# Optimization experiments

Hardware: AMD Instinct MI355X
Metric: run time of the kernel (lower is better)

The kernel has to match this reference:

```python
import jax, jax.numpy as jnp
import numpy as np

N = 100000   # nodes
E = 1600000  # edges (before self-loops)
F = 128      # num_features
H = 128      # hidden_dim
EPS = 1e-5   # BatchNorm eps


def setup_inputs() -> dict:
    key = jax.random.key(0)
    ks = jax.random.split(key, 8)
    x = jax.random.normal(ks[0], (N, F), dtype=jnp.float32)
    edge_index = jax.random.randint(ks[1], (2, E), 0, N, dtype=jnp.int64)

    def lin(k, din, dout):
        s = 1.0 / np.sqrt(din)
        kw, kb = jax.random.split(k)
        W = jax.random.uniform(kw, (din, dout), jnp.float32, -s, s)
        b = jax.random.uniform(kb, (dout,), jnp.float32, -s, s)
        return W, b

    W1, b1 = lin(ks[2], F, H)
    W2, b2 = lin(ks[3], H, H)
    W3, b3 = lin(ks[4], H, H)
    Wc, bc = lin(ks[5], H, 2)

    def bn_params():
        return (jnp.ones((H,), jnp.float32), jnp.zeros((H,), jnp.float32),
                jnp.zeros((H,), jnp.float32), jnp.ones((H,), jnp.float32))

    g1, be1, rm1, rv1 = bn_params()
    g2, be2, rm2, rv2 = bn_params()
    g3, be3, rm3, rv3 = bn_params()

    return {"x": x, "edge_index": edge_index,
            "W1": W1, "b1": b1, "W2": W2, "b2": b2, "W3": W3, "b3": b3,
            "g1": g1, "be1": be1, "rm1": rm1, "rv1": rv1,
            "g2": g2, "be2": be2, "rm2": rm2, "rv2": rv2,
            "g3": g3, "be3": be3, "rm3": rm3, "rv3": rv3,
            "Wc": Wc, "bc": bc}


def _gcn_norm(edge_index, num_nodes):
    # add self-loops, compute symmetric normalization (PyG GCNConv default)
    loop = jnp.arange(num_nodes, dtype=edge_index.dtype)
    src = jnp.concatenate([edge_index[0], loop])
    dst = jnp.concatenate([edge_index[1], loop])
    deg = jax.ops.segment_sum(jnp.ones_like(dst, dtype=jnp.float32), dst,
                              num_segments=num_nodes)
    dinv = jnp.where(deg > 0, jax.lax.rsqrt(deg), 0.0)
    norm = dinv[src] * dinv[dst]  # [E+N]
    return src, dst, norm


def _gcn_conv(x, W, b, src, dst, norm, num_nodes):
    h = x @ W                              # [N, H] linear first
    msg = h[src] * norm[:, None]           # gather + scale  [E+N, H]
    out = jax.ops.segment_sum(msg, dst, num_segments=num_nodes)  # scatter-add
    return out + b


def _bn_eval(x, g, be, rm, rv):
    return (x - rm) * jax.lax.rsqrt(rv + EPS) * g + be


def reference(x, edge_index,
              W1, b1, W2, b2, W3, b3,
              g1, be1, rm1, rv1,
              g2, be2, rm2, rv2,
              g3, be3, rm3, rv3,
              Wc, bc):
    n = x.shape[0]
    src, dst, norm = _gcn_norm(edge_index, n)
    h = _gcn_conv(x, W1, b1, src, dst, norm, n)
    h = _bn_eval(jax.nn.relu(h), g1, be1, rm1, rv1)
    # dropout: identity in eval mode
    h = _gcn_conv(h, W2, b2, src, dst, norm, n)
    h = _bn_eval(jax.nn.relu(h), g2, be2, rm2, rv2)
    h = _gcn_conv(h, W3, b3, src, dst, norm, n)
    h = _bn_eval(jax.nn.relu(h), g3, be3, rm3, rv3)
    return h @ Wc + bc  # [N, 2]
```

## Files before the change

### kernel.cpp

```cpp
#include <hip/hip_runtime.h>
#include <hip/hip_fp16.h>

#define BN_EPS 1e-5f
#define CHUNK 4096

typedef _Float16 half8 __attribute__((ext_vector_type(8)));
typedef float f32x4 __attribute__((ext_vector_type(4)));

__device__ __forceinline__ float4 f4zero() { return make_float4(0.f, 0.f, 0.f, 0.f); }


__global__ __launch_bounds__(256) void k_bucket_hist(const int* __restrict__ dst,
                                                     int* __restrict__ tableT,
                                                     int nA, int nbuck, int e) {
    __shared__ int h[1024];
    int blk = blockIdx.x, tid = threadIdx.x;
    for (int k = tid; k < 1024; k += 256) h[k] = 0;
    __syncthreads();
    int base = blk * CHUNK;
    if (base + CHUNK <= e && (e & 3) == 0) {
        const int4* d4 = (const int4*)(dst + base);
#pragma unroll
        for (int t = 0; t < 4; ++t) {
            int4 d = d4[t * 256 + tid];
            atomicAdd(&h[d.x >> 8], 1);
            atomicAdd(&h[d.y >> 8], 1);
            atomicAdd(&h[d.z >> 8], 1);
            atomicAdd(&h[d.w >> 8], 1);
        }
    } else {
        for (int i = base + tid; i < e && i < base + CHUNK; i += 256)
            atomicAdd(&h[dst[i] >> 8], 1);
    }
    __syncthreads();
    for (int k = tid; k < nbuck; k += 256)
        tableT[(size_t)k * nA + blk] = h[k];
}

__global__ __launch_bounds__(256) void k_bucket_scatter(const int* __restrict__ src,
                                                        const int* __restrict__ dst,
                                                        const int* __restrict__ tableT,
                                                        int2* __restrict__ bed,
                                                        int nA, int nbuck, int e) {
    __shared__ int cur[1024];
    int blk = blockIdx.x, tid = threadIdx.x;
    for (int k = tid; k < nbuck; k += 256)
        cur[k] = tableT[(size_t)k * nA + blk];
    __syncthreads();
    int base = blk * CHUNK;
    if (base + CHUNK <= e && (e & 3) == 0) {
        const int4* s4 = (const int4*)(src + base);
        const int4* d4 = (const int4*)(dst + base);
#pragma unroll
        for (int t = 0; t < 4; ++t) {
            int4 s = s4[t * 256 + tid];
            int4 d = d4[t * 256 + tid];
            int p0 = atomicAdd(&cur[d.x >> 8], 1); bed[p0] = make_int2(s.x, d.x);
            int p1 = atomicAdd(&cur[d.y >> 8], 1); bed[p1] = make_int2(s.y, d.y);
            int p2 = atomicAdd(&cur[d.z >> 8], 1); bed[p2] = make_int2(s.z, d.z);
            int p3 = atomicAdd(&cur[d.w >> 8], 1); bed[p3] = make_int2(s.w, d.w);
        }
    } else {
        for (int i = base + tid; i < e && i < base + CHUNK; i += 256) {
            int d = dst[i];
            int p = atomicAdd(&cur[d >> 8], 1);
            bed[p] = make_int2(src[i], d);
        }
    }
}

__global__ __launch_bounds__(256) void k_bucket_rank(const int2* __restrict__ bed,
                                                     const int* __restrict__ tableT,
                                                     int* __restrict__ brank,
                                                     int* __restrict__ counts,
                                                     int nA, int nbuck, int n, int e) {
    __shared__ int lcnt[256];
    int b = blockIdx.x, tid = threadIdx.x;
    lcnt[tid] = 0;
    __syncthreads();
    int start = tableT[(size_t)b * nA];
    int end = (b + 1 < nbuck) ? tableT[(size_t)(b + 1) * nA] : e;
    for (int i = start + tid; i < end; i += 256) {
        int2 q = bed[i];
        brank[i] = atomicAdd(&lcnt[q.y & 255], 1);
    }
    __syncthreads();
    int node = (b << 8) + tid;
    if (node < n) counts[node] = lcnt[tid];
}

__global__ __launch_bounds__(256) void k_dinv(const int* __restrict__ counts,
                                              float* __restrict__ dinv, int n) {
    int i = blockIdx.x * 256 + threadIdx.x;
    if (i < n) dinv[i] = rsqrtf((float)(counts[i] + 1));
}

template <bool PAD8>
__global__ __launch_bounds__(1024) void k_scan_block(const int* __restrict__ counts,
                                                     int* __restrict__ offs,
                                                     int* __restrict__ partials, int len) {
    __shared__ int s[1024];
    int t = threadIdx.x;
    int gid = blockIdx.x * 1024 + t;
    int c = (gid < len) ? counts[gid] : 0;
    int v = PAD8 ? ((c + 7) & ~7) : c;
    int x = v;
    s[t] = x;
    __syncthreads();
    for (int d = 1; d < 1024; d <<= 1) {
        int y = (t >= d) ? s[t - d] : 0;
        __syncthreads();
        x += y;
        s[t] = x;
        __syncthreads();
    }
    if (gid < len) offs[gid] = x - v;
    if (t == 1023) partials[blockIdx.x] = x;
}

__global__ __launch_bounds__(1024) void k_scan_partials(int* __restrict__ partials, int nb) {
    __shared__ int s[1024];
    int t = threadIdx.x;
    int v = (t < nb) ? partials[t] : 0;
    int x = v;
    s[t] = x;
    __syncthreads();
    for (int d = 1; d < 1024; d <<= 1) {
        int y = (t >= d) ? s[t - d] : 0;
        __syncthreads();
        x += y;
        s[t] = x;
        __syncthreads();
    }
    if (t < nb) partials[t] = x - v;
    if (t == nb - 1) partials[nb] = x;
}

__global__ __launch_bounds__(256) void k_scan_add(int* __restrict__ offs,
                                                  const int* __restrict__ partials, int len) {
    int gid = blockIdx.x * 256 + threadIdx.x;
    if (gid < len) offs[gid] += partials[gid >> 10];
    if (gid == 0) offs[len] = partials[(len + 1023) >> 10];
}

__global__ __launch_bounds__(256) void k_fill(int4* __restrict__ er4, int val, int m4) {
    int i = blockIdx.x * 256 + threadIdx.x;
    if (i < m4) er4[i] = make_int4(val, val, val, val);
}

__global__ __launch_bounds__(256) void k_place2(const int2* __restrict__ bed,
                                                const int* __restrict__ brank,
                                                const int* __restrict__ offs,
                                                int* __restrict__ er, int e) {
    int i = (blockIdx.x * 256 + threadIdx.x) * 2;
    if (i + 1 < e) {
        int4 q = *(const int4*)(bed + i);
        int2 r = *(const int2*)(brank + i);
        er[offs[q.y] + r.x] = q.x;
        er[offs[q.w] + r.y] = q.z;
    } else if (i < e) {
        int2 q = bed[i];
        er[offs[q.y] + brank[i]] = q.x;
    }
}


__global__ __launch_bounds__(256) void k_packW(const float* __restrict__ W,
                                               _Float16* __restrict__ out) {
    int t = blockIdx.x * 256 + threadIdx.x;
    if (t >= 2048) return;
    int kc = t >> 9;
    int rem = t & 511;
    int ct = rem >> 6;
    int lane = rem & 63;
    int q = lane >> 4;
    int col = ct * 16 + (lane & 15);
    half8 h;
#pragma unroll
    for (int j = 0; j < 8; ++j)
        h[j] = (_Float16)W[(kc * 32 + q * 8 + j) * 128 + col];
    *(half8*)(out + (size_t)t * 8) = h;
}


template <bool AF32>
__global__ __launch_bounds__(256) void k_gemm_mfma(const void* __restrict__ Av,
                                                   const _Float16* __restrict__ pW,
                                                   const float* __restrict__ dinv,
                                                   uint4* __restrict__ C, int n) {
    __shared__ char smem[32768];
    uint4* sW = (uint4*)smem;
    int tid = threadIdx.x;

    {
        const uint4* gW = (const uint4*)pW;
#pragma unroll
        for (int i = 0; i < 8; ++i) sW[tid + 256 * i] = gW[tid + 256 * i];
    }
    __syncthreads();

    int wave = tid >> 6, lane = tid & 63;
    int quad = lane >> 4, l16 = lane & 15;
    int row0 = blockIdx.x * 64 + wave * 16;
    int arow = row0 + l16;
    int arowc = (arow < n) ? arow : (n - 1);

    half8 af[4];
    if (AF32) {
        const float* A = (const float*)Av + (size_t)arowc * 128 + quad * 8;
#pragma unroll
        for (int kc = 0; kc < 4; ++kc) {
            float4 lo = *(const float4*)(A + kc * 32);
            float4 hi = *(const float4*)(A + kc * 32 + 4);
            half8 h;
            h[0] = (_Float16)lo.x; h[1] = (_Float16)lo.y;
            h[2] = (_Float16)lo.z; h[3] = (_Float16)lo.w;
            h[4] = (_Float16)hi.x; h[5] = (_Float16)hi.y;
            h[6] = (_Float16)hi.z; h[7] = (_Float16)hi.w;
            af[kc] = h;
        }
    } else {
        const _Float16* A = (const _Float16*)Av + (size_t)arowc * 128 + quad * 8;
#pragma unroll
        for (int kc = 0; kc < 4; ++kc)
            af[kc] = *(const half8*)(A + kc * 32);
    }

    f32x4 acc[8];
#pragma unroll
    for (int ct = 0; ct < 8; ++ct) acc[ct] = (f32x4){0.f, 0.f, 0.f, 0.f};

#pragma unroll
    for (int kc = 0; kc < 4; ++kc) {
#pragma unroll
        for (int ct = 0; ct < 8; ++ct) {
            half8 bf = *(half8*)&sW[(kc * 8 + ct) * 64 + lane];
            acc[ct] = __builtin_amdgcn_mfma_f32_16x16x32_f16(af[kc], bf, acc[ct], 0, 0, 0);
        }
    }

    __syncthreads();

    _Float16* eb = (_Float16*)smem + wave * 16 * 136;
    float dv[4];
#pragma unroll
    for (int r = 0; r < 4; ++r) {
        int rr = row0 + quad * 4 + r;
        dv[r] = dinv[(rr < n) ? rr : (n - 1)];
    }
#pragma unroll
    for (int ct = 0; ct < 8; ++ct)
#pragma unroll
        for (int r = 0; r < 4; ++r)
            eb[(quad * 4 + r) * 136 + ct * 16 + l16] = (_Float16)(acc[ct][r] * dv[r]);

#pragma unroll
    for (int i = 0; i < 4; ++i) {
        int linear = i * 64 + lane;
        int r = linear >> 4, c = linear & 15;
        uint4 v = *(uint4*)((char*)eb + r * 272 + c * 16);
        int row = row0 + r;
        if (row < n) C[(size_t)row * 16 + c] = v;
    }
}


__device__ __forceinline__ void acc_row(float4& acc, uint2 q) {
    float2 f01 = __half22float2(*(__half2*)&q.x);
    float2 f23 = __half22float2(*(__half2*)&q.y);
    acc.x += f01.x; acc.y += f01.y; acc.z += f23.x; acc.w += f23.y;
}

template <bool FUSE_CLS>
__global__ __launch_bounds__(256) void k_aggregate(const uint2* __restrict__ Ah,
                                                   const int* __restrict__ offs,
                                                   const int* __restrict__ er,
                                                   const float* __restrict__ dinv,
                                                   const float* __restrict__ bias,
                                                   const float* __restrict__ g,
                                                   const float* __restrict__ be,
                                                   const float* __restrict__ rm,
                                                   const float* __restrict__ rv,
                                                   uint2* __restrict__ Hout,
                                                   const float* __restrict__ Wc,
                                                   const float* __restrict__ bc,
                                                   float* __restrict__ out, int n) {
    int lane = threadIdx.x & 31;
    int node = blockIdx.x * 8 + (threadIdx.x >> 5);
    if (node >= n) return;

    float4 acc = f4zero();
    acc_row(acc, Ah[node * 32 + lane]);

    int e0 = offs[node], e1 = offs[node + 1];
    for (int e = e0; e < e1; e += 8) {
        int4 ra = *(const int4*)(er + e);
        int4 rb = *(const int4*)(er + e + 4);
        uint2 v0 = Ah[ra.x * 32 + lane];
        uint2 v1 = Ah[ra.y * 32 + lane];
        uint2 v2 = Ah[ra.z * 32 + lane];
        uint2 v3 = Ah[ra.w * 32 + lane];
        uint2 v4 = Ah[rb.x * 32 + lane];
        uint2 v5 = Ah[rb.y * 32 + lane];
        uint2 v6 = Ah[rb.z * 32 + lane];
        uint2 v7 = Ah[rb.w * 32 + lane];
        acc_row(acc, v0); acc_row(acc, v1); acc_row(acc, v2); acc_row(acc, v3);
        acc_row(acc, v4); acc_row(acc, v5); acc_row(acc, v6); acc_row(acc, v7);
    }

    float di = dinv[node];
    acc.x *= di; acc.y *= di; acc.z *= di; acc.w *= di;

    float4 b4  = ((const float4*)bias)[lane];
    float4 g4  = ((const float4*)g)[lane];
    float4 be4 = ((const float4*)be)[lane];
    float4 rm4 = ((const float4*)rm)[lane];
    float4 rv4 = ((const float4*)rv)[lane];

    float4 o;
    float v;
    v = fmaxf(acc.x + b4.x, 0.f); o.x = (v - rm4.x) * rsqrtf(rv4.x + BN_EPS) * g4.x + be4.x;
    v = fmaxf(acc.y + b4.y, 0.f); o.y = (v - rm4.y) * rsqrtf(rv4.y + BN_EPS) * g4.y + be4.y;
    v = fmaxf(acc.z + b4.z, 0.f); o.z = (v - rm4.z) * rsqrtf(rv4.z + BN_EPS) * g4.z + be4.z;
    v = fmaxf(acc.w + b4.w, 0.f); o.w = (v - rm4.w) * rsqrtf(rv4.w + BN_EPS) * g4.w + be4.w;

    if (!FUSE_CLS) {
        __half2 p0 = __floats2half2_rn(o.x, o.y);
        __half2 p1 = __floats2half2_rn(o.z, o.w);
        uint2 u;
        u.x = *(unsigned int*)&p0;
        u.y = *(unsigned int*)&p1;
        Hout[node * 32 + lane] = u;
    } else {
        const float4* Wv = (const float4*)Wc;
        float4 w01 = Wv[2 * lane];
        float4 w23 = Wv[2 * lane + 1];
        float p0 = o.x * w01.x + o.y * w01.z + o.z * w23.x + o.w * w23.z;
        float p1 = o.x * w01.y + o.y * w01.w + o.z * w23.y + o.w * w23.w;
#pragma unroll
        for (int d = 16; d >= 1; d >>= 1) {
            p0 += __shfl_down(p0, d, 32);
            p1 += __shfl_down(p1, d, 32);
        }
        if (lane == 0) {
            out[node * 2 + 0] = p0 + bc[0];
            out[node * 2 + 1] = p1 + bc[1];
        }
    }
}


extern "C" void kernel_launch(void* const* d_in, const int* in_sizes, int n_in,
                              void* d_out, int out_size, void* d_ws, size_t ws_size,
                              hipStream_t stream) {
    const float* x   = (const float*)d_in[0];
    const int*   ei  = (const int*)d_in[1];
    const float* W1  = (const float*)d_in[2];
    const float* b1  = (const float*)d_in[3];
    const float* W2  = (const float*)d_in[4];
    const float* b2  = (const float*)d_in[5];
    const float* W3  = (const float*)d_in[6];
    const float* b3  = (const float*)d_in[7];
    const float* g1  = (const float*)d_in[8];
    const float* be1 = (const float*)d_in[9];
    const float* rm1 = (const float*)d_in[10];
    const float* rv1 = (const float*)d_in[11];
    const float* g2  = (const float*)d_in[12];
    const float* be2 = (const float*)d_in[13];
    const float* rm2 = (const float*)d_in[14];
    const float* rv2 = (const float*)d_in[15];
    const float* g3  = (const float*)d_in[16];
    const float* be3 = (const float*)d_in[17];
    const float* rm3 = (const float*)d_in[18];
    const float* rv3 = (const float*)d_in[19];
    const float* Wc  = (const float*)d_in[20];
    const float* bc  = (const float*)d_in[21];
    float* out = (float*)d_out;

    int n = in_sizes[0] / 128;
    int e = in_sizes[1] / 2;
    const int* src = ei;
    const int* dst = ei + e;

    char* ws = (char*)d_ws;
    size_t off = 0;
    auto alloc = [&](size_t bytes) -> char* {
        char* p = ws + off;
        off += (bytes + 255) & ~(size_t)255;
        return p;
    };
    int erCap = e + 8 * n;
    uint2*     bufA   = (uint2*)alloc((size_t)(n + 1) * 128 * 2);
    char*      bufH   = (char*) alloc((size_t)n * 128 * 4);
    float*     dinv   = (float*)alloc((size_t)n * 4);
    int*       counts = (int*)  alloc((size_t)n * 4);
    int*       offs   = (int*)  alloc((size_t)(n + 1) * 4);
    int*       parts  = (int*)  alloc(8192);
    int*       er     = (int*)  alloc((size_t)erCap * 4);
    _Float16*  pW     = (_Float16*)alloc(3 * 16384 * 2);
    (void)ws_size; (void)n_in; (void)out_size;

    int nA    = (e + CHUNK - 1) / CHUNK;
    int nbuck = (n + 255) >> 8;
    int tlen  = nbuck * nA;
    {
        char* p = bufH + (size_t)n * 128 * 2;
        size_t po = 0;
        auto palloc = [&](size_t bytes) -> char* {
            char* q = p + po;
            po += (bytes + 255) & ~(size_t)255;
            return q;
        };
        int2* bed    = (int2*)palloc((size_t)e * 8);
        int*  brank  = (int*) palloc((size_t)e * 4);
        int*  tableT = (int*) palloc((size_t)(tlen + 1) * 4);

        hipMemsetAsync(bufA + (size_t)n * 32, 0, 256, stream);

        int gN  = (n + 255) / 256;
        int nb  = (n + 1023) / 1024;
        int nbT = (tlen + 1023) / 1024;
        int m4  = erCap / 4;

        k_packW<<<8, 256, 0, stream>>>(W1, pW);
        k_packW<<<8, 256, 0, stream>>>(W2, pW + 16384);
        k_packW<<<8, 256, 0, stream>>>(W3, pW + 32768);
        k_bucket_hist<<<nA, 256, 0, stream>>>(dst, tableT, nA, nbuck, e);
        k_scan_block<false><<<nbT, 1024, 0, stream>>>(tableT, tableT, parts, tlen);
        k_scan_partials<<<1, 1024, 0, stream>>>(parts, nbT);
        k_scan_add<<<(tlen + 255) / 256, 256, 0, stream>>>(tableT, parts, tlen);
        k_bucket_scatter<<<nA, 256, 0, stream>>>(src, dst, tableT, bed, nA, nbuck, e);
        k_bucket_rank<<<nbuck, 256, 0, stream>>>(bed, tableT, brank, counts, nA, nbuck, n, e);
        k_dinv<<<gN, 256, 0, stream>>>(counts, dinv, n);
        k_scan_block<true><<<nb, 1024, 0, stream>>>(counts, offs, parts, n);
        k_scan_partials<<<1, 1024, 0, stream>>>(parts, nb);
        k_scan_add<<<gN, 256, 0, stream>>>(offs, parts, n);
        k_fill<<<(m4 + 255) / 256, 256, 0, stream>>>((int4*)er, n, m4);
        k_place2<<<((e + 1) / 2 + 255) / 256, 256, 0, stream>>>(bed, brank, offs, er, e);
    }

    int gGemm = (n + 63) / 64;
    int gAgg  = (n + 7) / 8;

    k_gemm_mfma<true><<<gGemm, 256, 0, stream>>>(x, pW, dinv, (uint4*)bufA, n);
    k_aggregate<false><<<gAgg, 256, 0, stream>>>(bufA, offs, er, dinv,
                                                 b1, g1, be1, rm1, rv1, (uint2*)bufH,
                                                 nullptr, nullptr, nullptr, n);

    k_gemm_mfma<false><<<gGemm, 256, 0, stream>>>(bufH, pW + 16384, dinv, (uint4*)bufA, n);
    k_aggregate<false><<<gAgg, 256, 0, stream>>>(bufA, offs, er, dinv,
                                                 b2, g2, be2, rm2, rv2, (uint2*)bufH,
                                                 nullptr, nullptr, nullptr, n);

    k_gemm_mfma<false><<<gGemm, 256, 0, stream>>>(bufH, pW + 32768, dinv, (uint4*)bufA, n);
    k_aggregate<true><<<gAgg, 256, 0, stream>>>(bufA, offs, er, dinv,
                                                b3, g3, be3, rm3, rv3, nullptr,
                                                Wc, bc, out, n);
}
```

Baseline: 412.2 us.

## Widen aggregate gathers to 16-byte loads with half-wave edge split, shrink buckets

The aggregation kernel now has each 16-lane half-wave load full 16-byte fp16 chunks. The two halves work on alternating edges, and their partial sums are combined with a cross-half shuffle. Accumulation uses fdot2 to convert fp16 to fp32 while adding. Separately, the bucket sort uses 128-node buckets and smaller chunks, and the dinv computation is folded into the rank kernel, which removes one launch. The wider gathers should cut per-edge memory instructions, at the cost of an extra reduction and idle lanes for the self-row and the output store.

```diff
diff --git a/kernel.cpp b/kernel.cpp
--- a/kernel.cpp
+++ b/kernel.cpp
@@ -2,9 +2,11 @@
 #include <hip/hip_fp16.h>
 
 #define BN_EPS 1e-5f
-#define CHUNK 4096
+#define CHUNK 2048
+#define BBITS 7
 
 typedef _Float16 half8 __attribute__((ext_vector_type(8)));
+typedef _Float16 half2v __attribute__((ext_vector_type(2)));
 typedef float f32x4 __attribute__((ext_vector_type(4)));
 
 __device__ __forceinline__ float4 f4zero() { return make_float4(0.f, 0.f, 0.f, 0.f); }
@@ -21,16 +23,16 @@
     if (base + CHUNK <= e && (e & 3) == 0) {
         const int4* d4 = (const int4*)(dst + base);
 #pragma unroll
-        for (int t = 0; t < 4; ++t) {
+        for (int t = 0; t < CHUNK / 1024; ++t) {
             int4 d = d4[t * 256 + tid];
-            atomicAdd(&h[d.x >> 8], 1);
-            atomicAdd(&h[d.y >> 8], 1);
-            atomicAdd(&h[d.z >> 8], 1);
-            atomicAdd(&h[d.w >> 8], 1);
+            atomicAdd(&h[d.x >> BBITS], 1);
+            atomicAdd(&h[d.y >> BBITS], 1);
+            atomicAdd(&h[d.z >> BBITS], 1);
+            atomicAdd(&h[d.w >> BBITS], 1);
         }
     } else {
         for (int i = base + tid; i < e && i < base + CHUNK; i += 256)
-            atomicAdd(&h[dst[i] >> 8], 1);
+            atomicAdd(&h[dst[i] >> BBITS], 1);
     }
     __syncthreads();
     for (int k = tid; k < nbuck; k += 256)
@@ -52,18 +54,18 @@
         const int4* s4 = (const int4*)(src + base);
         const int4* d4 = (const int4*)(dst + base);
 #pragma unroll
-        for (int t = 0; t < 4; ++t) {
+        for (int t = 0; t < CHUNK / 1024; ++t) {
             int4 s = s4[t * 256 + tid];
             int4 d = d4[t * 256 + tid];
-            int p0 = atomicAdd(&cur[d.x >> 8], 1); bed[p0] = make_int2(s.x, d.x);
-            int p1 = atomicAdd(&cur[d.y >> 8], 1); bed[p1] = make_int2(s.y, d.y);
-            int p2 = atomicAdd(&cur[d.z >> 8], 1); bed[p2] = make_int2(s.z, d.z);
-            int p3 = atomicAdd(&cur[d.w >> 8], 1); bed[p3] = make_int2(s.w, d.w);
+            int p0 = atomicAdd(&cur[d.x >> BBITS], 1); bed[p0] = make_int2(s.x, d.x);
+            int p1 = atomicAdd(&cur[d.y >> BBITS], 1); bed[p1] = make_int2(s.y, d.y);
+            int p2 = atomicAdd(&cur[d.z >> BBITS], 1); bed[p2] = make_int2(s.z, d.z);
+            int p3 = atomicAdd(&cur[d.w >> BBITS], 1); bed[p3] = make_int2(s.w, d.w);
         }
     } else {
         for (int i = base + tid; i < e && i < base + CHUNK; i += 256) {
             int d = dst[i];
-            int p = atomicAdd(&cur[d >> 8], 1);
+            int p = atomicAdd(&cur[d >> BBITS], 1);
             bed[p] = make_int2(src[i], d);
         }
     }
@@ -73,26 +75,27 @@
                                                      const int* __restrict__ tableT,
                                                      int* __restrict__ brank,
                                                      int* __restrict__ counts,
+                                                     float* __restrict__ dinv,
                                                      int nA, int nbuck, int n, int e) {
-    __shared__ int lcnt[256];
+    __shared__ int lcnt[128];
     int b = blockIdx.x, tid = threadIdx.x;
-    lcnt[tid] = 0;
+    if (tid < 128) lcnt[tid] = 0;
     __syncthreads();
     int start = tableT[(size_t)b * nA];
     int end = (b + 1 < nbuck) ? tableT[(size_t)(b + 1) * nA] : e;
     for (int i = start + tid; i < end; i += 256) {
         int2 q = bed[i];
-        brank[i] = atomicAdd(&lcnt[q.y & 255], 1);
-    }
-    __syncthreads();
-    int node = (b << 8) + tid;
-    if (node < n) counts[node] = lcnt[tid];
-}
-
-__global__ __launch_bounds__(256) void k_dinv(const int* __restrict__ counts,
-                                              float* __restrict__ dinv, int n) {
-    int i = blockIdx.x * 256 + threadIdx.x;
-    if (i < n) dinv[i] = rsqrtf((float)(counts[i] + 1));
+        brank[i] = atomicAdd(&lcnt[q.y & ((1 << BBITS) - 1)], 1);
+    }
+    __syncthreads();
+    if (tid < 128) {
+        int node = (b << BBITS) + tid;
+        if (node < n) {
+            int c = lcnt[tid];
+            counts[node] = c;
+            dinv[node] = rsqrtf((float)(c + 1));
+        }
+    }
 }
 
 template <bool PAD8>
@@ -265,14 +268,20 @@
 }
 
 
-__device__ __forceinline__ void acc_row(float4& acc, uint2 q) {
-    float2 f01 = __half22float2(*(__half2*)&q.x);
-    float2 f23 = __half22float2(*(__half2*)&q.y);
-    acc.x += f01.x; acc.y += f01.y; acc.z += f23.x; acc.w += f23.y;
+__device__ __forceinline__ void accum8(float* acc, uint4 q) {
+    const half2v b0 = {(_Float16)1.0f, (_Float16)0.0f};
+    const half2v b1 = {(_Float16)0.0f, (_Float16)1.0f};
+    unsigned int u[4] = {q.x, q.y, q.z, q.w};
+#pragma unroll
+    for (int k = 0; k < 4; ++k) {
+        half2v h = *(half2v*)&u[k];
+        acc[2 * k + 0] = __builtin_amdgcn_fdot2(h, b0, acc[2 * k + 0], false);
+        acc[2 * k + 1] = __builtin_amdgcn_fdot2(h, b1, acc[2 * k + 1], false);
+    }
 }
 
 template <bool FUSE_CLS>
-__global__ __launch_bounds__(256) void k_aggregate(const uint2* __restrict__ Ah,
+__global__ __launch_bounds__(256) void k_aggregate(const uint4* __restrict__ Ah4,
                                                    const int* __restrict__ offs,
                                                    const int* __restrict__ er,
                                                    const float* __restrict__ dinv,
@@ -281,68 +290,88 @@
                                                    const float* __restrict__ be,
                                                    const float* __restrict__ rm,
                                                    const float* __restrict__ rv,
-                                                   uint2* __restrict__ Hout,
+                                                   uint4* __restrict__ Hout,
                                                    const float* __restrict__ Wc,
                                                    const float* __restrict__ bc,
                                                    float* __restrict__ out, int n) {
-    int lane = threadIdx.x & 31;
+    int lane32 = threadIdx.x & 31;
     int node = blockIdx.x * 8 + (threadIdx.x >> 5);
     if (node >= n) return;
-
-    float4 acc = f4zero();
-    acc_row(acc, Ah[node * 32 + lane]);
+    int sub = lane32 & 15;
+    bool hi = lane32 >= 16;
+
+    float acc[8];
+#pragma unroll
+    for (int j = 0; j < 8; ++j) acc[j] = 0.f;
+
+    {
+        uint4 qs = Ah4[(size_t)node * 16 + sub];
+        if (!hi) accum8(acc, qs);
+    }
 
     int e0 = offs[node], e1 = offs[node + 1];
     for (int e = e0; e < e1; e += 8) {
         int4 ra = *(const int4*)(er + e);
         int4 rb = *(const int4*)(er + e + 4);
-        uint2 v0 = Ah[ra.x * 32 + lane];
-        uint2 v1 = Ah[ra.y * 32 + lane];
-        uint2 v2 = Ah[ra.z * 32 + lane];
-        uint2 v3 = Ah[ra.w * 32 + lane];
-        uint2 v4 = Ah[rb.x * 32 + lane];
-        uint2 v5 = Ah[rb.y * 32 + lane];
-        uint2 v6 = Ah[rb.z * 32 + lane];
-        uint2 v7 = Ah[rb.w * 32 + lane];
-        acc_row(acc, v0); acc_row(acc, v1); acc_row(acc, v2); acc_row(acc, v3);
-        acc_row(acc, v4); acc_row(acc, v5); acc_row(acc, v6); acc_row(acc, v7);
-    }
+        int r0 = hi ? ra.y : ra.x;
+        int r1 = hi ? ra.w : ra.z;
+        int r2 = hi ? rb.y : rb.x;
+        int r3 = hi ? rb.w : rb.z;
+        uint4 q0 = Ah4[(size_t)r0 * 16 + sub];
+        uint4 q1 = Ah4[(size_t)r1 * 16 + sub];
+        uint4 q2 = Ah4[(size_t)r2 * 16 + sub];
+        uint4 q3 = Ah4[(size_t)r3 * 16 + sub];
+        accum8(acc, q0); accum8(acc, q1); accum8(acc, q2); accum8(acc, q3);
+    }
+
+#pragma unroll
+    for (int j = 0; j < 8; ++j) acc[j] += __shfl_xor(acc[j], 16, 32);
 
     float di = dinv[node];
-    acc.x *= di; acc.y *= di; acc.z *= di; acc.w *= di;
-
-    float4 b4  = ((const float4*)bias)[lane];
-    float4 g4  = ((const float4*)g)[lane];
-    float4 be4 = ((const float4*)be)[lane];
-    float4 rm4 = ((const float4*)rm)[lane];
-    float4 rv4 = ((const float4*)rv)[lane];
-
-    float4 o;
-    float v;
-    v = fmaxf(acc.x + b4.x, 0.f); o.x = (v - rm4.x) * rsqrtf(rv4.x + BN_EPS) * g4.x + be4.x;
-    v = fmaxf(acc.y + b4.y, 0.f); o.y = (v - rm4.y) * rsqrtf(rv4.y + BN_EPS) * g4.y + be4.y;
-    v = fmaxf(acc.z + b4.z, 0.f); o.z = (v - rm4.z) * rsqrtf(rv4.z + BN_EPS) * g4.z + be4.z;
-    v = fmaxf(acc.w + b4.w, 0.f); o.w = (v - rm4.w) * rsqrtf(rv4.w + BN_EPS) * g4.w + be4.w;
+    const float4* b4 = (const float4*)bias;
+    const float4* g4 = (const float4*)g;
+    const float4* be4 = (const float4*)be;
+    const float4* rm4 = (const float4*)rm;
+    const float4* rv4 = (const float4*)rv;
+
+    float o[8];
+#pragma unroll
+    for (int h = 0; h < 2; ++h) {
+        float4 bb = b4[sub * 2 + h], gg = g4[sub * 2 + h], ee = be4[sub * 2 + h];
+        float4 mm = rm4[sub * 2 + h], vv = rv4[sub * 2 + h];
+        float v;
+        v = fmaxf(acc[4 * h + 0] * di + bb.x, 0.f); o[4 * h + 0] = (v - mm.x) * rsqrtf(vv.x + BN_EPS) * gg.x + ee.x;
+        v = fmaxf(acc[4 * h + 1] * di + bb.y, 0.f); o[4 * h + 1] = (v - mm.y) * rsqrtf(vv.y + BN_EPS) * gg.y + ee.y;
+        v = fmaxf(acc[4 * h + 2] * di + bb.z, 0.f); o[4 * h + 2] = (v - mm.z) * rsqrtf(vv.z + BN_EPS) * gg.z + ee.z;
+        v = fmaxf(acc[4 * h + 3] * di + bb.w, 0.f); o[4 * h + 3] = (v - mm.w) * rsqrtf(vv.w + BN_EPS) * gg.w + ee.w;
+    }
 
     if (!FUSE_CLS) {
-        __half2 p0 = __floats2half2_rn(o.x, o.y);
-        __half2 p1 = __floats2half2_rn(o.z, o.w);
-        uint2 u;
-        u.x = *(unsigned int*)&p0;
-        u.y = *(unsigned int*)&p1;
-        Hout[node * 32 + lane] = u;
+        if (!hi) {
+            __half2 p0 = __floats2half2_rn(o[0], o[1]);
+            __half2 p1 = __floats2half2_rn(o[2], o[3]);
+            __half2 p2 = __floats2half2_rn(o[4], o[5]);
+            __half2 p3 = __floats2half2_rn(o[6], o[7]);
+            uint4 u;
+            u.x = *(unsigned int*)&p0; u.y = *(unsigned int*)&p1;
+            u.z = *(unsigned int*)&p2; u.w = *(unsigned int*)&p3;
+            Hout[(size_t)node * 16 + sub] = u;
+        }
     } else {
         const float4* Wv = (const float4*)Wc;
-        float4 w01 = Wv[2 * lane];
-        float4 w23 = Wv[2 * lane + 1];
-        float p0 = o.x * w01.x + o.y * w01.z + o.z * w23.x + o.w * w23.z;
-        float p1 = o.x * w01.y + o.y * w01.w + o.z * w23.y + o.w * w23.w;
-#pragma unroll
-        for (int d = 16; d >= 1; d >>= 1) {
-            p0 += __shfl_down(p0, d, 32);
-            p1 += __shfl_down(p1, d, 32);
-        }
-        if (lane == 0) {
+        float p0 = 0.f, p1 = 0.f;
+#pragma unroll
+        for (int k = 0; k < 4; ++k) {
+            float4 w = Wv[sub * 4 + k];
+            p0 += o[2 * k] * w.x + o[2 * k + 1] * w.z;
+            p1 += o[2 * k] * w.y + o[2 * k + 1] * w.w;
+        }
+#pragma unroll
+        for (int d = 8; d >= 1; d >>= 1) {
+            p0 += __shfl_down(p0, d, 16);
+            p1 += __shfl_down(p1, d, 16);
+        }
+        if (lane32 == 0) {
             out[node * 2 + 0] = p0 + bc[0];
             out[node * 2 + 1] = p1 + bc[1];
         }
@@ -401,7 +430,7 @@
     (void)ws_size; (void)n_in; (void)out_size;
 
     int nA    = (e + CHUNK - 1) / CHUNK;
-    int nbuck = (n + 255) >> 8;
+    int nbuck = (n + (1 << BBITS) - 1) >> BBITS;
     int tlen  = nbuck * nA;
     {
         char* p = bufH + (size_t)n * 128 * 2;
@@ -430,8 +459,7 @@
         k_scan_partials<<<1, 1024, 0, stream>>>(parts, nbT);
         k_scan_add<<<(tlen + 255) / 256, 256, 0, stream>>>(tableT, parts, tlen);
         k_bucket_scatter<<<nA, 256, 0, stream>>>(src, dst, tableT, bed, nA, nbuck, e);
-        k_bucket_rank<<<nbuck, 256, 0, stream>>>(bed, tableT, brank, counts, nA, nbuck, n, e);
-        k_dinv<<<gN, 256, 0, stream>>>(counts, dinv, n);
+        k_bucket_rank<<<nbuck, 256, 0, stream>>>(bed, tableT, brank, counts, dinv, nA, nbuck, n, e);
         k_scan_block<true><<<nb, 1024, 0, stream>>>(counts, offs, parts, n);
         k_scan_partials<<<1, 1024, 0, stream>>>(parts, nb);
         k_scan_add<<<gN, 256, 0, stream>>>(offs, parts, n);
@@ -443,17 +471,17 @@
     int gAgg  = (n + 7) / 8;
 
     k_gemm_mfma<true><<<gGemm, 256, 0, stream>>>(x, pW, dinv, (uint4*)bufA, n);
-    k_aggregate<false><<<gAgg, 256, 0, stream>>>(bufA, offs, er, dinv,
-                                                 b1, g1, be1, rm1, rv1, (uint2*)bufH,
+    k_aggregate<false><<<gAgg, 256, 0, stream>>>((const uint4*)bufA, offs, er, dinv,
+                                                 b1, g1, be1, rm1, rv1, (uint4*)bufH,
                                                  nullptr, nullptr, nullptr, n);
 
     k_gemm_mfma<false><<<gGemm, 256, 0, stream>>>(bufH, pW + 16384, dinv, (uint4*)bufA, n);
-    k_aggregate<false><<<gAgg, 256, 0, stream>>>(bufA, offs, er, dinv,
-                                                 b2, g2, be2, rm2, rv2, (uint2*)bufH,
+    k_aggregate<false><<<gAgg, 256, 0, stream>>>((const uint4*)bufA, offs, er, dinv,
+                                                 b2, g2, be2, rm2, rv2, (uint4*)bufH,
                                                  nullptr, nullptr, nullptr, n);
 
     k_gemm_mfma<false><<<gGemm, 256, 0, stream>>>(bufH, pW + 32768, dinv, (uint4*)bufA, n);
-    k_aggregate<true><<<gAgg, 256, 0, stream>>>(bufA, offs, er, dinv,
+    k_aggregate<true><<<gAgg, 256, 0, stream>>>((const uint4*)bufA, offs, er, dinv,
                                                 b3, g3, be3, rm3, rv3, nullptr,
                                                 Wc, bc, out, n);
 }
```

Result: slower. 433.8 us (+5.3%).

## Fuse CSR-build preprocessing into fewer kernels with per-bucket local scans

Applied to the files above, without the earlier changes.

Restructures the graph preprocessing pipeline. Weight packing is merged into the histogram kernel, and bucket size shrinks to 128 nodes. The rank kernel now also computes dinv and a padded local prefix scan per bucket, so the global node scan becomes a small scan over bucket totals. The fill, place and zeroing steps are merged into one finalize kernel. This cuts the launch count roughly in half and drops the full-array padding fill, at the cost of more histogram buckets and a serial per-node padding loop.

```diff
diff --git a/kernel.cpp b/kernel.cpp
--- a/kernel.cpp
+++ b/kernel.cpp
@@ -3,6 +3,7 @@
 
 #define BN_EPS 1e-5f
 #define CHUNK 4096
+#define BBITS 7
 
 typedef _Float16 half8 __attribute__((ext_vector_type(8)));
 typedef float f32x4 __attribute__((ext_vector_type(4)));
@@ -10,32 +11,95 @@
 __device__ __forceinline__ float4 f4zero() { return make_float4(0.f, 0.f, 0.f, 0.f); }
 
 
-__global__ __launch_bounds__(256) void k_bucket_hist(const int* __restrict__ dst,
-                                                     int* __restrict__ tableT,
-                                                     int nA, int nbuck, int e) {
+__global__ __launch_bounds__(256) void k_pack_hist(const float* __restrict__ W1,
+                                                   const float* __restrict__ W2,
+                                                   const float* __restrict__ W3,
+                                                   _Float16* __restrict__ pW,
+                                                   const int* __restrict__ dst,
+                                                   int* __restrict__ tableT,
+                                                   int nA, int nbuck, int e) {
     __shared__ int h[1024];
-    int blk = blockIdx.x, tid = threadIdx.x;
+    int tid = threadIdx.x;
+    if (blockIdx.x < 24) {
+        int t = blockIdx.x * 256 + tid;
+        int wi = t >> 11;
+        int tt = t & 2047;
+        const float* W = (wi == 0) ? W1 : ((wi == 1) ? W2 : W3);
+        int kc = tt >> 9;
+        int rem = tt & 511;
+        int ct = rem >> 6;
+        int lane = rem & 63;
+        int q = lane >> 4;
+        int col = ct * 16 + (lane & 15);
+        half8 hh;
+#pragma unroll
+        for (int j = 0; j < 8; ++j)
+            hh[j] = (_Float16)W[(kc * 32 + q * 8 + j) * 128 + col];
+        *(half8*)(pW + (size_t)t * 8) = hh;
+        return;
+    }
+    int blk = blockIdx.x - 24;
     for (int k = tid; k < 1024; k += 256) h[k] = 0;
     __syncthreads();
     int base = blk * CHUNK;
     if (base + CHUNK <= e && (e & 3) == 0) {
         const int4* d4 = (const int4*)(dst + base);
 #pragma unroll
-        for (int t = 0; t < 4; ++t) {
+        for (int t = 0; t < CHUNK / 1024; ++t) {
             int4 d = d4[t * 256 + tid];
-            atomicAdd(&h[d.x >> 8], 1);
-            atomicAdd(&h[d.y >> 8], 1);
-            atomicAdd(&h[d.z >> 8], 1);
-            atomicAdd(&h[d.w >> 8], 1);
+            atomicAdd(&h[d.x >> BBITS], 1);
+            atomicAdd(&h[d.y >> BBITS], 1);
+            atomicAdd(&h[d.z >> BBITS], 1);
+            atomicAdd(&h[d.w >> BBITS], 1);
         }
     } else {
         for (int i = base + tid; i < e && i < base + CHUNK; i += 256)
-            atomicAdd(&h[dst[i] >> 8], 1);
+            atomicAdd(&h[dst[i] >> BBITS], 1);
     }
     __syncthreads();
     for (int k = tid; k < nbuck; k += 256)
         tableT[(size_t)k * nA + blk] = h[k];
 }
+
+
+__global__ __launch_bounds__(1024) void k_scan_block(const int* __restrict__ in,
+                                                     int* __restrict__ outp,
+                                                     int* __restrict__ partials, int len) {
+    __shared__ int s[1024];
+    int t = threadIdx.x;
+    int gid = blockIdx.x * 1024 + t;
+    int v = (gid < len) ? in[gid] : 0;
+    int x = v;
+    s[t] = x;
+    __syncthreads();
+    for (int d = 1; d < 1024; d <<= 1) {
+        int y = (t >= d) ? s[t - d] : 0;
+        __syncthreads();
+        x += y;
+        s[t] = x;
+        __syncthreads();
+    }
+    if (gid < len) outp[gid] = x - v;
+    if (t == 1023) partials[blockIdx.x] = x;
+}
+
+__global__ __launch_bounds__(256) void k_scan_addp(int* __restrict__ data,
+                                                   const int* __restrict__ partials, int len) {
+    __shared__ int red[256];
+    int tid = threadIdx.x;
+    int K = blockIdx.x >> 2;
+    int s = 0;
+    for (int t = tid; t < K; t += 256) s += partials[t];
+    red[tid] = s;
+    __syncthreads();
+    for (int d = 128; d > 0; d >>= 1) {
+        if (tid < d) red[tid] += red[tid + d];
+        __syncthreads();
+    }
+    int gid = blockIdx.x * 256 + tid;
+    if (gid < len) data[gid] += red[0];
+}
+
 
 __global__ __launch_bounds__(256) void k_bucket_scatter(const int* __restrict__ src,
                                                         const int* __restrict__ dst,
@@ -52,58 +116,74 @@
         const int4* s4 = (const int4*)(src + base);
         const int4* d4 = (const int4*)(dst + base);
 #pragma unroll
-        for (int t = 0; t < 4; ++t) {
+        for (int t = 0; t < CHUNK / 1024; ++t) {
             int4 s = s4[t * 256 + tid];
             int4 d = d4[t * 256 + tid];
-            int p0 = atomicAdd(&cur[d.x >> 8], 1); bed[p0] = make_int2(s.x, d.x);
-            int p1 = atomicAdd(&cur[d.y >> 8], 1); bed[p1] = make_int2(s.y, d.y);
-            int p2 = atomicAdd(&cur[d.z >> 8], 1); bed[p2] = make_int2(s.z, d.z);
-            int p3 = atomicAdd(&cur[d.w >> 8], 1); bed[p3] = make_int2(s.w, d.w);
+            int p0 = atomicAdd(&cur[d.x >> BBITS], 1); bed[p0] = make_int2(s.x, d.x);
+            int p1 = atomicAdd(&cur[d.y >> BBITS], 1); bed[p1] = make_int2(s.y, d.y);
+            int p2 = atomicAdd(&cur[d.z >> BBITS], 1); bed[p2] = make_int2(s.z, d.z);
+            int p3 = atomicAdd(&cur[d.w >> BBITS], 1); bed[p3] = make_int2(s.w, d.w);
         }
     } else {
         for (int i = base + tid; i < e && i < base + CHUNK; i += 256) {
             int d = dst[i];
-            int p = atomicAdd(&cur[d >> 8], 1);
+            int p = atomicAdd(&cur[d >> BBITS], 1);
             bed[p] = make_int2(src[i], d);
         }
     }
 }
+
 
 __global__ __launch_bounds__(256) void k_bucket_rank(const int2* __restrict__ bed,
                                                      const int* __restrict__ tableT,
                                                      int* __restrict__ brank,
                                                      int* __restrict__ counts,
+                                                     float* __restrict__ dinv,
+                                                     int* __restrict__ localOff,
+                                                     int* __restrict__ btot,
                                                      int nA, int nbuck, int n, int e) {
-    __shared__ int lcnt[256];
+    __shared__ int lcnt[128];
+    __shared__ int lscan[128];
     int b = blockIdx.x, tid = threadIdx.x;
-    lcnt[tid] = 0;
+    if (tid < 128) lcnt[tid] = 0;
     __syncthreads();
     int start = tableT[(size_t)b * nA];
     int end = (b + 1 < nbuck) ? tableT[(size_t)(b + 1) * nA] : e;
     for (int i = start + tid; i < end; i += 256) {
         int2 q = bed[i];
-        brank[i] = atomicAdd(&lcnt[q.y & 255], 1);
-    }
-    __syncthreads();
-    int node = (b << 8) + tid;
-    if (node < n) counts[node] = lcnt[tid];
-}
-
-__global__ __launch_bounds__(256) void k_dinv(const int* __restrict__ counts,
-                                              float* __restrict__ dinv, int n) {
-    int i = blockIdx.x * 256 + threadIdx.x;
-    if (i < n) dinv[i] = rsqrtf((float)(counts[i] + 1));
-}
-
-template <bool PAD8>
-__global__ __launch_bounds__(1024) void k_scan_block(const int* __restrict__ counts,
-                                                     int* __restrict__ offs,
-                                                     int* __restrict__ partials, int len) {
+        brank[i] = atomicAdd(&lcnt[q.y & 127], 1);
+    }
+    __syncthreads();
+    int padded = 0;
+    if (tid < 128) {
+        padded = (lcnt[tid] + 7) & ~7;
+        lscan[tid] = padded;
+    }
+    __syncthreads();
+    for (int d = 1; d < 128; d <<= 1) {
+        int y = (tid < 128 && tid >= d) ? lscan[tid - d] : 0;
+        __syncthreads();
+        if (tid < 128) lscan[tid] += y;
+        __syncthreads();
+    }
+    if (tid < 128) {
+        int node = (b << BBITS) + tid;
+        if (node < n) {
+            int c = lcnt[tid];
+            counts[node] = c;
+            dinv[node] = rsqrtf((float)(c + 1));
+            localOff[node] = lscan[tid] - padded;
+        }
+        if (tid == 127) btot[b] = lscan[127];
+    }
+}
+
+
+__global__ __launch_bounds__(1024) void k_scan_buckets(const int* __restrict__ btot,
+                                                       int* __restrict__ bucketBase, int nbuck) {
     __shared__ int s[1024];
     int t = threadIdx.x;
-    int gid = blockIdx.x * 1024 + t;
-    int c = (gid < len) ? counts[gid] : 0;
-    int v = PAD8 ? ((c + 7) & ~7) : c;
+    int v = (t < nbuck) ? btot[t] : 0;
     int x = v;
     s[t] = x;
     __syncthreads();
@@ -114,72 +194,44 @@
         s[t] = x;
         __syncthreads();
     }
-    if (gid < len) offs[gid] = x - v;
-    if (t == 1023) partials[blockIdx.x] = x;
-}
-
-__global__ __launch_bounds__(1024) void k_scan_partials(int* __restrict__ partials, int nb) {
-    __shared__ int s[1024];
-    int t = threadIdx.x;
-    int v = (t < nb) ? partials[t] : 0;
-    int x = v;
-    s[t] = x;
-    __syncthreads();
-    for (int d = 1; d < 1024; d <<= 1) {
-        int y = (t >= d) ? s[t - d] : 0;
-        __syncthreads();
-        x += y;
-        s[t] = x;
-        __syncthreads();
-    }
-    if (t < nb) partials[t] = x - v;
-    if (t == nb - 1) partials[nb] = x;
-}
-
-__global__ __launch_bounds__(256) void k_scan_add(int* __restrict__ offs,
-                                                  const int* __restrict__ partials, int len) {
-    int gid = blockIdx.x * 256 + threadIdx.x;
-    if (gid < len) offs[gid] += partials[gid >> 10];
-    if (gid == 0) offs[len] = partials[(len + 1023) >> 10];
-}
-
-__global__ __launch_bounds__(256) void k_fill(int4* __restrict__ er4, int val, int m4) {
-    int i = blockIdx.x * 256 + threadIdx.x;
-    if (i < m4) er4[i] = make_int4(val, val, val, val);
-}
-
-__global__ __launch_bounds__(256) void k_place2(const int2* __restrict__ bed,
-                                                const int* __restrict__ brank,
-                                                const int* __restrict__ offs,
-                                                int* __restrict__ er, int e) {
-    int i = (blockIdx.x * 256 + threadIdx.x) * 2;
-    if (i + 1 < e) {
-        int4 q = *(const int4*)(bed + i);
-        int2 r = *(const int2*)(brank + i);
-        er[offs[q.y] + r.x] = q.x;
-        er[offs[q.w] + r.y] = q.z;
-    } else if (i < e) {
-        int2 q = bed[i];
-        er[offs[q.y] + brank[i]] = q.x;
-    }
-}
-
-
-__global__ __launch_bounds__(256) void k_packW(const float* __restrict__ W,
-                                               _Float16* __restrict__ out) {
-    int t = blockIdx.x * 256 + threadIdx.x;
-    if (t >= 2048) return;
-    int kc = t >> 9;
-    int rem = t & 511;
-    int ct = rem >> 6;
-    int lane = rem & 63;
-    int q = lane >> 4;
-    int col = ct * 16 + (lane & 15);
-    half8 h;
-#pragma unroll
-    for (int j = 0; j < 8; ++j)
-        h[j] = (_Float16)W[(kc * 32 + q * 8 + j) * 128 + col];
-    *(half8*)(out + (size_t)t * 8) = h;
+    if (t < nbuck) bucketBase[t] = x - v;
+    if (t == nbuck - 1) bucketBase[nbuck] = x;
+}
+
+
+__global__ __launch_bounds__(256) void k_finalize(const int* __restrict__ counts,
+                                                  const int* __restrict__ localOff,
+                                                  const int* __restrict__ bucketBase,
+                                                  int* __restrict__ offs,
+                                                  int* __restrict__ er,
+                                                  const int2* __restrict__ bed,
+                                                  const int* __restrict__ brank,
+                                                  unsigned int* __restrict__ bufAzero,
+                                                  int n, int e, int gN, int nbuck) {
+    int tid = threadIdx.x;
+    if (blockIdx.x < gN) {
+        int node = blockIdx.x * 256 + tid;
+        if (node < n) {
+            int c = counts[node];
+            int o = bucketBase[node >> BBITS] + localOff[node];
+            offs[node] = o;
+            int pc = (c + 7) & ~7;
+            for (int j = c; j < pc; ++j) er[o + j] = n;
+        }
+        if (node == 0) offs[n] = bucketBase[nbuck];
+        if (blockIdx.x == 0 && tid < 64) bufAzero[tid] = 0u;
+    } else {
+        int i = ((blockIdx.x - gN) * 256 + tid) * 2;
+        if (i + 1 < e) {
+            int4 q = *(const int4*)(bed + i);
+            int2 r = *(const int2*)(brank + i);
+            er[bucketBase[q.y >> BBITS] + localOff[q.y] + r.x] = q.x;
+            er[bucketBase[q.w >> BBITS] + localOff[q.w] + r.y] = q.z;
+        } else if (i < e) {
+            int2 q = bed[i];
+            er[bucketBase[q.y >> BBITS] + localOff[q.y] + brank[i]] = q.x;
+        }
+    }
 }
 
 
@@ -290,20 +342,20 @@
     if (node >= n) return;
 
     float4 acc = f4zero();
-    acc_row(acc, Ah[node * 32 + lane]);
+    acc_row(acc, Ah[(size_t)node * 32 + lane]);
 
     int e0 = offs[node], e1 = offs[node + 1];
     for (int e = e0; e < e1; e += 8) {
         int4 ra = *(const int4*)(er + e);
         int4 rb = *(const int4*)(er + e + 4);
-        uint2 v0 = Ah[ra.x * 32 + lane];
-        uint2 v1 = Ah[ra.y * 32 + lane];
-        uint2 v2 = Ah[ra.z * 32 + lane];
-        uint2 v3 = Ah[ra.w * 32 + lane];
-        uint2 v4 = Ah[rb.x * 32 + lane];
-        uint2 v5 = Ah[rb.y * 32 + lane];
-        uint2 v6 = Ah[rb.z * 32 + lane];
-        uint2 v7 = Ah[rb.w * 32 + lane];
+        uint2 v0 = Ah[(size_t)ra.x * 32 + lane];
+        uint2 v1 = Ah[(size_t)ra.y * 32 + lane];
+        uint2 v2 = Ah[(size_t)ra.z * 32 + lane];
+        uint2 v3 = Ah[(size_t)ra.w * 32 + lane];
+        uint2 v4 = Ah[(size_t)rb.x * 32 + lane];
+        uint2 v5 = Ah[(size_t)rb.y * 32 + lane];
+        uint2 v6 = Ah[(size_t)rb.z * 32 + lane];
+        uint2 v7 = Ah[(size_t)rb.w * 32 + lane];
         acc_row(acc, v0); acc_row(acc, v1); acc_row(acc, v2); acc_row(acc, v3);
         acc_row(acc, v4); acc_row(acc, v5); acc_row(acc, v6); acc_row(acc, v7);
     }
@@ -330,7 +382,7 @@
         uint2 u;
         u.x = *(unsigned int*)&p0;
         u.y = *(unsigned int*)&p1;
-        Hout[node * 32 + lane] = u;
+        Hout[(size_t)node * 32 + lane] = u;
     } else {
         const float4* Wv = (const float4*)Wc;
         float4 w01 = Wv[2 * lane];
@@ -389,71 +441,57 @@
         off += (bytes + 255) & ~(size_t)255;
         return p;
     };
+    int nA    = (e + CHUNK - 1) / CHUNK;
+    int nbuck = (n + (1 << BBITS) - 1) >> BBITS;
+    int tlen  = nbuck * nA;
     int erCap = e + 8 * n;
-    uint2*     bufA   = (uint2*)alloc((size_t)(n + 1) * 128 * 2);
-    char*      bufH   = (char*) alloc((size_t)n * 128 * 4);
-    float*     dinv   = (float*)alloc((size_t)n * 4);
-    int*       counts = (int*)  alloc((size_t)n * 4);
-    int*       offs   = (int*)  alloc((size_t)(n + 1) * 4);
-    int*       parts  = (int*)  alloc(8192);
-    int*       er     = (int*)  alloc((size_t)erCap * 4);
-    _Float16*  pW     = (_Float16*)alloc(3 * 16384 * 2);
+
+    char*      bufA     = (char*) alloc((size_t)(n + 1) * 256);
+    char*      bufH     = (char*) alloc((size_t)n * 256);
+    float*     dinv     = (float*)alloc((size_t)n * 4);
+    int*       counts   = (int*)  alloc((size_t)n * 4);
+    int*       offs     = (int*)  alloc((size_t)(n + 1) * 4);
+    int*       localOff = (int*)  alloc((size_t)n * 4);
+    int*       btot     = (int*)  alloc((size_t)(nbuck + 1) * 4);
+    int*       bktBase  = (int*)  alloc((size_t)(nbuck + 1) * 4);
+    int*       tableT   = (int*)  alloc((size_t)(tlen + 1) * 4);
+    int*       parts    = (int*)  alloc(8192);
+    int*       er       = (int*)  alloc((size_t)erCap * 4);
+    _Float16*  pW       = (_Float16*)alloc(3 * 16384 * 2);
     (void)ws_size; (void)n_in; (void)out_size;
 
-    int nA    = (e + CHUNK - 1) / CHUNK;
-    int nbuck = (n + 255) >> 8;
-    int tlen  = nbuck * nA;
-    {
-        char* p = bufH + (size_t)n * 128 * 2;
-        size_t po = 0;
-        auto palloc = [&](size_t bytes) -> char* {
-            char* q = p + po;
-            po += (bytes + 255) & ~(size_t)255;
-            return q;
-        };
-        int2* bed    = (int2*)palloc((size_t)e * 8);
-        int*  brank  = (int*) palloc((size_t)e * 4);
-        int*  tableT = (int*) palloc((size_t)(tlen + 1) * 4);
-
-        hipMemsetAsync(bufA + (size_t)n * 32, 0, 256, stream);
-
-        int gN  = (n + 255) / 256;
-        int nb  = (n + 1023) / 1024;
-        int nbT = (tlen + 1023) / 1024;
-        int m4  = erCap / 4;
-
-        k_packW<<<8, 256, 0, stream>>>(W1, pW);
-        k_packW<<<8, 256, 0, stream>>>(W2, pW + 16384);
-        k_packW<<<8, 256, 0, stream>>>(W3, pW + 32768);
-        k_bucket_hist<<<nA, 256, 0, stream>>>(dst, tableT, nA, nbuck, e);
-        k_scan_block<false><<<nbT, 1024, 0, stream>>>(tableT, tableT, parts, tlen);
-        k_scan_partials<<<1, 1024, 0, stream>>>(parts, nbT);
-        k_scan_add<<<(tlen + 255) / 256, 256, 0, stream>>>(tableT, parts, tlen);
-        k_bucket_scatter<<<nA, 256, 0, stream>>>(src, dst, tableT, bed, nA, nbuck, e);
-        k_bucket_rank<<<nbuck, 256, 0, stream>>>(bed, tableT, brank, counts, nA, nbuck, n, e);
-        k_dinv<<<gN, 256, 0, stream>>>(counts, dinv, n);
-        k_scan_block<true><<<nb, 1024, 0, stream>>>(counts, offs, parts, n);
-        k_scan_partials<<<1, 1024, 0, stream>>>(parts, nb);
-        k_scan_add<<<gN, 256, 0, stream>>>(offs, parts, n);
-        k_fill<<<(m4 + 255) / 256, 256, 0, stream>>>((int4*)er, n, m4);
-        k_place2<<<((e + 1) / 2 + 255) / 256, 256, 0, stream>>>(bed, brank, offs, er, e);
-    }
+    int2* bed   = (int2*)bufH;
+    int*  brank = (int*)(bufH + (size_t)e * 8);
+
+    int gN  = (n + 255) / 256;
+    int nbT = (tlen + 1023) / 1024;
+
+    k_pack_hist<<<24 + nA, 256, 0, stream>>>(W1, W2, W3, pW, dst, tableT, nA, nbuck, e);
+    k_scan_block<<<nbT, 1024, 0, stream>>>(tableT, tableT, parts, tlen);
+    k_scan_addp<<<(tlen + 255) / 256, 256, 0, stream>>>(tableT, parts, tlen);
+    k_bucket_scatter<<<nA, 256, 0, stream>>>(src, dst, tableT, bed, nA, nbuck, e);
+    k_bucket_rank<<<nbuck, 256, 0, stream>>>(bed, tableT, brank, counts, dinv, localOff,
+                                             btot, nA, nbuck, n, e);
+    k_scan_buckets<<<1, 1024, 0, stream>>>(btot, bktBase, nbuck);
+    int gP = gN + (e / 2 + 255) / 256 + 1;
+    k_finalize<<<gP, 256, 0, stream>>>(counts, localOff, bktBase, offs, er, bed, brank,
+                                       (unsigned int*)(bufA + (size_t)n * 256), n, e, gN, nbuck);
 
     int gGemm = (n + 63) / 64;
     int gAgg  = (n + 7) / 8;
 
     k_gemm_mfma<true><<<gGemm, 256, 0, stream>>>(x, pW, dinv, (uint4*)bufA, n);
-    k_aggregate<false><<<gAgg, 256, 0, stream>>>(bufA, offs, er, dinv,
+    k_aggregate<false><<<gAgg, 256, 0, stream>>>((const uint2*)bufA, offs, er, dinv,
                                                  b1, g1, be1, rm1, rv1, (uint2*)bufH,
                                                  nullptr, nullptr, nullptr, n);
 
     k_gemm_mfma<false><<<gGemm, 256, 0, stream>>>(bufH, pW + 16384, dinv, (uint4*)bufA, n);
-    k_aggregate<false><<<gAgg, 256, 0, stream>>>(bufA, offs, er, dinv,
+    k_aggregate<false><<<gAgg, 256, 0, stream>>>((const uint2*)bufA, offs, er, dinv,
                                                  b2, g2, be2, rm2, rv2, (uint2*)bufH,
                                                  nullptr, nullptr, nullptr, n);
 
     k_gemm_mfma<false><<<gGemm, 256, 0, stream>>>(bufH, pW + 32768, dinv, (uint4*)bufA, n);
-    k_aggregate<true><<<gAgg, 256, 0, stream>>>(bufA, offs, er, dinv,
+    k_aggregate<true><<<gAgg, 256, 0, stream>>>((const uint2*)bufA, offs, er, dinv,
                                                 b3, g3, be3, rm3, rv3, nullptr,
                                                 Wc, bc, out, n);
 }
```

After: 394.7 us. 1.04x faster.
